# Performance work log

Measured on AMD Instinct MI355X. Metric: run time of the kernel, lower is better.

The kernel has to match this reference:

```python
import jax, jax.numpy as jnp
import numpy as np

ALPHA = 0.25
GAMMA = 2.0
EDGE_W = 1.0
NODE_W = 1.0

N = 200_000
E = 12_800_000
N_GRAPHS = 16
N_INST = 1000


def setup_inputs() -> dict:
    key = jax.random.key(0)
    k1, k2, k3, k4, k5 = jax.random.split(key, 5)
    edge_logits = jax.random.normal(k1, (E,), dtype=jnp.float32)
    node_logits = jax.random.normal(k2, (N,), dtype=jnp.float32)
    batch = jnp.sort(jax.random.randint(k3, (N,), 0, N_GRAPHS, dtype=jnp.int64) if jax.config.read('jax_enable_x64') else jax.random.randint(k3, (N,), 0, N_GRAPHS, dtype=jnp.int32))
    point_instances = jax.random.randint(k4, (N,), 0, N_INST, dtype=jnp.int32)
    edge_index = jax.random.randint(k5, (2, E), 0, N, dtype=jnp.int32)
    return {"edge_logits": edge_logits, "node_logits": node_logits,
            "batch": batch, "point_instances": point_instances,
            "edge_index": edge_index}


def _bce_with_logits(x, t):
    # numerically stable elementwise BCE-with-logits (reduction='none')
    return jnp.maximum(x, 0.0) - x * t + jnp.log1p(jnp.exp(-jnp.abs(x)))


def _sigmoid_focal_loss(x, t, alpha, gamma):
    # torchvision.ops.sigmoid_focal_loss, reduction='mean'
    p = jax.nn.sigmoid(x)
    ce = _bce_with_logits(x, t)
    p_t = p * t + (1.0 - p) * (1.0 - t)
    loss = ce * (1.0 - p_t) ** gamma
    alpha_t = alpha * t + (1.0 - alpha) * (1.0 - t)
    return jnp.mean(alpha_t * loss)


def _accuracy(x, t):
    # sigmoid > 0.5 -> 1 else 0 (note: == 0.5 maps to 0, as in the original)
    pred = (jax.nn.sigmoid(x) > 0.5).astype(x.dtype)
    return jnp.mean((pred == t).astype(jnp.float32))


def reference(edge_logits, node_logits, batch, point_instances, edge_index):
    src, dst = edge_index[0], edge_index[1]
    pi_s = point_instances[src]
    pi_d = point_instances[dst]
    # edge-wise equivalent of the original N x N mask gathered at edge_index:
    # same instance AND same graph AND both instances nonzero
    same = (pi_s == pi_d) & (batch[src] == batch[dst]) & (pi_s != 0) & (pi_d != 0)
    edge_targets = same.astype(jnp.float32)  # [E]

    edge_loss = _sigmoid_focal_loss(edge_logits, edge_targets, ALPHA, GAMMA)
    edge_acc = _accuracy(edge_logits, edge_targets)

    node_targets = (point_instances != 0).astype(jnp.float32)  # [N]
    node_loss = _sigmoid_focal_loss(node_logits, node_targets, ALPHA, GAMMA)
    node_acc = _accuracy(node_logits, node_targets)

    loss = EDGE_W * edge_loss + NODE_W * node_loss
    return loss, edge_loss, node_loss, edge_acc, node_acc
```

## Files before the change

### kernel.cpp

```cpp
#include <hip/hip_runtime.h>
#include <limits.h>


typedef int   iv4 __attribute__((ext_vector_type(4)));
typedef float fv4 __attribute__((ext_vector_type(4)));

#define MAX_PART 4096

__device__ __forceinline__ float focal_term(float x, int t) {
    float y = t ? -x : x;
    float e = __expf(-fabsf(y));
    float ce = fmaxf(y, 0.f) + __logf(1.f + e);
    float inv = __builtin_amdgcn_rcpf(1.f + e);
    float sg = (y >= 0.f) ? inv : e * inv;
    float w = t ? 0.25f : 0.75f;
    return w * ce * sg * sg;
}

__device__ __forceinline__ float acc_term(float x, int t) {
    return ((x > 0.f) == (t != 0)) ? 1.f : 0.f;
}

__device__ __forceinline__ void block_store2(float v0, float v1, float2* part) {
#pragma unroll
    for (int off = 32; off > 0; off >>= 1) {
        v0 += __shfl_down(v0, off, 64);
        v1 += __shfl_down(v1, off, 64);
    }
    __shared__ float s0[8], s1[8];
    int wave = threadIdx.x >> 6;
    int lane = threadIdx.x & 63;
    if (lane == 0) { s0[wave] = v0; s1[wave] = v1; }
    __syncthreads();
    if (threadIdx.x == 0) {
        int nw = blockDim.x >> 6;
        float t0 = 0.f, t1 = 0.f;
        for (int w = 0; w < nw; ++w) { t0 += s0[w]; t1 += s1[w]; }
        part[blockIdx.x] = make_float2(t0, t1);
    }
}

__device__ __forceinline__ void block_store4(float v0, float v1, float v2,
                                             float v3, float4* part) {
#pragma unroll
    for (int off = 32; off > 0; off >>= 1) {
        v0 += __shfl_down(v0, off, 64);
        v1 += __shfl_down(v1, off, 64);
        v2 += __shfl_down(v2, off, 64);
        v3 += __shfl_down(v3, off, 64);
    }
    __shared__ float s[4][8];
    int wave = threadIdx.x >> 6;
    int lane = threadIdx.x & 63;
    if (lane == 0) { s[0][wave] = v0; s[1][wave] = v1;
                     s[2][wave] = v2; s[3][wave] = v3; }
    __syncthreads();
    if (threadIdx.x == 0) {
        int nw = blockDim.x >> 6;
        float t0 = 0.f, t1 = 0.f, t2 = 0.f, t3 = 0.f;
        for (int w = 0; w < nw; ++w) {
            t0 += s[0][w]; t1 += s[1][w]; t2 += s[2][w]; t3 += s[3][w];
        }
        part[blockIdx.x] = make_float4(t0, t1, t2, t3);
    }
}

__global__ void __launch_bounds__(256, 4)
node_e1_kernel(const float* __restrict__ nl,
               const int* __restrict__ batch,
               const int* __restrict__ pi,
               int N,
               const float* __restrict__ el, int E,
               unsigned short* __restrict__ key,
               int* __restrict__ bnd,
               float4* __restrict__ part) {
    int tid = blockIdx.x * blockDim.x + threadIdx.x;
    int nth = gridDim.x * blockDim.x;
    float nls = 0.f, nac = 0.f, els = 0.f, eac = 0.f;

    int C = N >> 3;
    const iv4* pi4 = reinterpret_cast<const iv4*>(pi);
    const iv4* b4  = reinterpret_cast<const iv4*>(batch);
    const fv4* nl4 = reinterpret_cast<const fv4*>(nl);
    for (int c = tid; c < C; c += nth) {
        int base = c << 3;
        iv4 p0 = pi4[(c << 1) + 0], p1 = pi4[(c << 1) + 1];
        iv4 b0 = b4[(c << 1) + 0],  b1 = b4[(c << 1) + 1];
        fv4 x0 = nl4[(c << 1) + 0], x1 = nl4[(c << 1) + 1];
        int pv[8] = {p0.x, p0.y, p0.z, p0.w, p1.x, p1.y, p1.z, p1.w};
        int bv[8] = {b0.x, b0.y, b0.z, b0.w, b1.x, b1.y, b1.z, b1.w};
        float xv[8] = {x0.x, x0.y, x0.z, x0.w, x1.x, x1.y, x1.z, x1.w};
        int bp = (base > 0) ? batch[base - 1] : -1;
        unsigned int kv[8];
#pragma unroll
        for (int j = 0; j < 8; ++j) {
            int p = pv[j];
            int t = (p != 0) ? 1 : 0;
            int b = bv[j];
            kv[j] = t ? (unsigned int)((b << 10) | p) : 0u;
            if (bp != b) {
                for (int k = bp + 1; k <= b; ++k) bnd[k] = base + j;
            }
            bp = b;
            nls += focal_term(xv[j], t);
            nac += acc_term(xv[j], t);
        }
        if (base + 8 == N) {
            for (int k = bv[7] + 1; k <= 16; ++k) bnd[k] = N;
        }
        iv4 kp;
        kp.x = (int)(kv[0] | (kv[1] << 16));
        kp.y = (int)(kv[2] | (kv[3] << 16));
        kp.z = (int)(kv[4] | (kv[5] << 16));
        kp.w = (int)(kv[6] | (kv[7] << 16));
        reinterpret_cast<iv4*>(key)[c] = kp;
    }
    if (tid == 0) {
        for (int i = C << 3; i < N; ++i) {
            int p = pi[i];
            int t = (p != 0) ? 1 : 0;
            int b = batch[i];
            key[i] = t ? (unsigned short)((b << 10) | p) : (unsigned short)0;
            if (i == 0) {
                for (int k = 0; k <= b; ++k) bnd[k] = 0;
            } else {
                int bp = batch[i - 1];
                for (int k = bp + 1; k <= b; ++k) bnd[k] = i;
            }
            if (i == N - 1) {
                for (int k = b + 1; k <= 16; ++k) bnd[k] = N;
            }
            float x = nl[i];
            nls += focal_term(x, t);
            nac += acc_term(x, t);
        }
    }

    int G16 = E >> 4;
    const fv4* el4 = reinterpret_cast<const fv4*>(el);
    for (int g = tid; g < G16; g += nth) {
        int base = g << 2;
        fv4 y0 = __builtin_nontemporal_load(el4 + base + 0);
        fv4 y1 = __builtin_nontemporal_load(el4 + base + 1);
        fv4 y2 = __builtin_nontemporal_load(el4 + base + 2);
        fv4 y3 = __builtin_nontemporal_load(el4 + base + 3);
        float xv[16] = {y0.x, y0.y, y0.z, y0.w, y1.x, y1.y, y1.z, y1.w,
                        y2.x, y2.y, y2.z, y2.w, y3.x, y3.y, y3.z, y3.w};
#pragma unroll
        for (int i = 0; i < 16; ++i) {
            els += focal_term(xv[i], 0);
            eac += acc_term(xv[i], 0);
        }
    }
    if (tid == 0) {
        for (int i = G16 << 4; i < E; ++i) {
            float x = el[i];
            els += focal_term(x, 0);
            eac += acc_term(x, 0);
        }
    }
    block_store4(nls, nac, els, eac, part);
}

__global__ void __launch_bounds__(256, 4)
edge_corr_kernel(const int* __restrict__ src,
                 const int* __restrict__ dst,
                 const float* __restrict__ el,
                 const unsigned short* __restrict__ key,
                 const int* __restrict__ bnd_g,
                 int E, float gscale,
                 float2* __restrict__ part) {
    __shared__ int bnd[17];
    if (threadIdx.x < 17) bnd[threadIdx.x] = bnd_g[threadIdx.x];
    __syncthreads();

    const int G16 = E >> 4;
    int tid = blockIdx.x * blockDim.x + threadIdx.x;
    int nth = gridDim.x * blockDim.x;
    float ls = 0.f, ac = 0.f;
    const iv4* src4 = reinterpret_cast<const iv4*>(src);
    const iv4* dst4 = reinterpret_cast<const iv4*>(dst);

    for (int g = tid; g < G16; g += nth) {
        int base = g << 2;
#pragma unroll
        for (int j = 0; j < 4; ++j) {
            iv4 s4 = __builtin_nontemporal_load(src4 + base + j);
            iv4 d4 = __builtin_nontemporal_load(dst4 + base + j);
            int ss[4] = {s4.x, s4.y, s4.z, s4.w};
            int dd[4] = {d4.x, d4.y, d4.z, d4.w};
#pragma unroll
            for (int k = 0; k < 4; ++k) {
                int s = ss[k], d = dd[k];
                int gg = (int)((float)s * gscale);
                gg = gg < 0 ? 0 : (gg > 15 ? 15 : gg);
                int lo = bnd[gg], hi = bnd[gg + 1];
                while (s < lo) { --gg; hi = lo; lo = bnd[gg]; }
                while (s >= hi) { ++gg; lo = hi; hi = bnd[gg + 1]; }
                if ((d >= lo) & (d < hi)) {
                    unsigned short ks = key[s];
                    unsigned short kd = key[d];
                    if ((ks == kd) & (ks != 0)) {
                        float x = el[(g << 4) + (j << 2) + k];
                        ls += focal_term(x, 1) - focal_term(x, 0);
                        ac += (x > 0.f) ? 1.f : -1.f;
                    }
                }
            }
        }
    }
    if (tid == 0) {
        for (int i = (G16 << 4); i < E; ++i) {
            int s = src[i], d = dst[i];
            int gg = (int)((float)s * gscale);
            gg = gg < 0 ? 0 : (gg > 15 ? 15 : gg);
            int lo = bnd[gg], hi = bnd[gg + 1];
            while (s < lo) { --gg; hi = lo; lo = bnd[gg]; }
            while (s >= hi) { ++gg; lo = hi; hi = bnd[gg + 1]; }
            if ((d >= lo) & (d < hi)) {
                unsigned short ks = key[s], kd = key[d];
                if ((ks == kd) & (ks != 0)) {
                    float x = el[i];
                    ls += focal_term(x, 1) - focal_term(x, 0);
                    ac += (x > 0.f) ? 1.f : -1.f;
                }
            }
        }
    }
    block_store2(ls, ac, part);
}

__global__ void node_atomic_kernel(const float* __restrict__ nl,
                                   const int* __restrict__ pi,
                                   int N, float* __restrict__ acc) {
    int stride = gridDim.x * blockDim.x;
    float ls = 0.f, ac = 0.f;
    for (int i = blockIdx.x * blockDim.x + threadIdx.x; i < N; i += stride) {
        int t = (pi[i] != 0) ? 1 : 0;
        float x = nl[i];
        ls += focal_term(x, t);
        ac += acc_term(x, t);
    }
#pragma unroll
    for (int off = 32; off > 0; off >>= 1) {
        ls += __shfl_down(ls, off, 64);
        ac += __shfl_down(ac, off, 64);
    }
    if ((threadIdx.x & 63) == 0) {
        atomicAdd(acc + 2, ls);
        atomicAdd(acc + 3, ac);
    }
}

__global__ void edge_kernel_direct(const float* __restrict__ el,
                                   const int* __restrict__ src,
                                   const int* __restrict__ dst,
                                   const int* __restrict__ batch,
                                   const int* __restrict__ pi,
                                   int E, float* __restrict__ acc) {
    int stride = gridDim.x * blockDim.x;
    float ls = 0.f, ac = 0.f;
    for (int i = blockIdx.x * blockDim.x + threadIdx.x; i < E; i += stride) {
        int ps = pi[src[i]], pd = pi[dst[i]];
        int t = (ps == pd) & (batch[src[i]] == batch[dst[i]]) & (ps != 0);
        float x = el[i];
        ls += focal_term(x, t);
        ac += acc_term(x, t);
    }
#pragma unroll
    for (int off = 32; off > 0; off >>= 1) {
        ls += __shfl_down(ls, off, 64);
        ac += __shfl_down(ac, off, 64);
    }
    if ((threadIdx.x & 63) == 0) {
        atomicAdd(acc + 0, ls);
        atomicAdd(acc + 1, ac);
    }
}

__global__ void finalize_kernel(const float* __restrict__ acc,
                                const float4* __restrict__ p1, int n1,
                                const float2* __restrict__ p2, int n2,
                                int use_part,
                                float* __restrict__ out, int E, int N) {
    if (use_part) {
        float nls = 0.f, nac = 0.f, els = 0.f, eac = 0.f;
        for (int i = threadIdx.x; i < n1; i += 256) {
            float4 p = p1[i];
            nls += p.x; nac += p.y; els += p.z; eac += p.w;
        }
        for (int i = threadIdx.x; i < n2; i += 256) {
            float2 p = p2[i];
            els += p.x; eac += p.y;
        }
#pragma unroll
        for (int off = 32; off > 0; off >>= 1) {
            nls += __shfl_down(nls, off, 64);
            nac += __shfl_down(nac, off, 64);
            els += __shfl_down(els, off, 64);
            eac += __shfl_down(eac, off, 64);
        }
        __shared__ float s[4][4];
        int wave = threadIdx.x >> 6;
        int lane = threadIdx.x & 63;
        if (lane == 0) { s[0][wave] = nls; s[1][wave] = nac;
                         s[2][wave] = els; s[3][wave] = eac; }
        __syncthreads();
        if (threadIdx.x == 0) {
            nls = 0.f; nac = 0.f; els = 0.f; eac = 0.f;
            for (int w = 0; w < 4; ++w) {
                nls += s[0][w]; nac += s[1][w];
                els += s[2][w]; eac += s[3][w];
            }
            float invE = 1.f / (float)E;
            float invN = 1.f / (float)N;
            float elm = els * invE, eam = eac * invE;
            float nlm = nls * invN, nam = nac * invN;
            out[0] = elm + nlm;
            out[1] = elm;
            out[2] = nlm;
            out[3] = eam;
            out[4] = nam;
        }
    } else if (threadIdx.x == 0) {
        float invE = 1.f / (float)E;
        float invN = 1.f / (float)N;
        float elm = acc[0] * invE;
        float eam = acc[1] * invE;
        float nlm = acc[2] * invN;
        float nam = acc[3] * invN;
        out[0] = elm + nlm;
        out[1] = elm;
        out[2] = nlm;
        out[3] = eam;
        out[4] = nam;
    }
}

extern "C" void kernel_launch(void* const* d_in, const int* in_sizes, int n_in,
                              void* d_out, int out_size, void* d_ws, size_t ws_size,
                              hipStream_t stream) {
    const float* edge_logits = (const float*)d_in[0];
    const float* node_logits = (const float*)d_in[1];
    const int*   batch       = (const int*)d_in[2];
    const int*   pinst       = (const int*)d_in[3];
    const int*   eidx        = (const int*)d_in[4];
    const int E = in_sizes[0];
    const int N = in_sizes[1];
    const int* src = eidx;
    const int* dst = eidx + E;
    float* out = (float*)d_out;

    float* acc = (float*)d_ws;
    int*   bnd = (int*)((char*)d_ws + 64);
    unsigned short* key = (unsigned short*)((char*)d_ws + 256);
    size_t key_end = 256 + (size_t)N * sizeof(unsigned short);
    size_t part_off = (key_end + 255) & ~(size_t)255;
    float4* part1 = (float4*)((char*)d_ws + part_off);
    float2* part2 = (float2*)(part1 + MAX_PART);
    size_t need_full = part_off + MAX_PART * (sizeof(float4) + sizeof(float2));

    const bool full = (ws_size >= need_full);
    const int block = 256;
    int C = N >> 3;
    int G16 = E >> 4;

    if (full) {
        int g1 = (G16 + block - 1) / block;
        int g1n = (C + block - 1) / block;
        if (g1n > g1) g1 = g1n;
        if (g1 < 1) g1 = 1;
        if (g1 > MAX_PART) g1 = MAX_PART;
        int g2 = (G16 + block - 1) / block;
        if (g2 < 1) g2 = 1;
        if (g2 > MAX_PART) g2 = MAX_PART;

        node_e1_kernel<<<g1, block, 0, stream>>>(node_logits, batch, pinst, N,
                                                 edge_logits, E, key, bnd, part1);
        float gscale = 16.0f / (float)N;
        edge_corr_kernel<<<g2, block, 0, stream>>>(src, dst, edge_logits, key,
                                                   bnd, E, gscale, part2);
        finalize_kernel<<<1, 256, 0, stream>>>(acc, part1, g1, part2, g2, 1,
                                               out, E, N);
    } else {
        (void)hipMemsetAsync(d_ws, 0, 16, stream);
        int ng = (N + block - 1) / block;
        if (ng > 2048) ng = 2048;
        node_atomic_kernel<<<ng, block, 0, stream>>>(node_logits, pinst, N, acc);
        int eg = (E + block - 1) / block;
        if (eg > 2048) eg = 2048;
        edge_kernel_direct<<<eg, block, 0, stream>>>(edge_logits, src, dst,
                                                     batch, pinst, E, acc);
        finalize_kernel<<<1, 256, 0, stream>>>(acc, part1, 0, part2, 0, 0,
                                               out, E, N);
    }
}
```

Before: 242.7 us.

## Drop packed key array, use wave-coalesced edge loads and deferred pi gathers

Removes the 16-bit packed key array written by the node kernel. The edge kernel now gathers point_instances directly, which is safe because the same-graph check is already done through the batch boundaries. Both edge loops switch from per-thread contiguous 64-byte chunks to wave-strided float4 loads, so each load instruction covers a contiguous 1 KB span per wave. The correction kernel first builds a bitmask of same-graph edges and then runs the pi gathers only for set bits, at the cost of 4-byte instead of 2-byte gathers and a larger register array per thread.

Result: faster. 202.5 us (-16.6%).

```diff
diff --git a/kernel.cpp b/kernel.cpp
--- a/kernel.cpp
+++ b/kernel.cpp
@@ -71,7 +71,6 @@
                const int* __restrict__ pi,
                int N,
                const float* __restrict__ el, int E,
-               unsigned short* __restrict__ key,
                int* __restrict__ bnd,
                float4* __restrict__ part) {
     int tid = blockIdx.x * blockDim.x + threadIdx.x;
@@ -91,13 +90,10 @@
         int bv[8] = {b0.x, b0.y, b0.z, b0.w, b1.x, b1.y, b1.z, b1.w};
         float xv[8] = {x0.x, x0.y, x0.z, x0.w, x1.x, x1.y, x1.z, x1.w};
         int bp = (base > 0) ? batch[base - 1] : -1;
-        unsigned int kv[8];
 #pragma unroll
         for (int j = 0; j < 8; ++j) {
-            int p = pv[j];
-            int t = (p != 0) ? 1 : 0;
+            int t = (pv[j] != 0) ? 1 : 0;
             int b = bv[j];
-            kv[j] = t ? (unsigned int)((b << 10) | p) : 0u;
             if (bp != b) {
                 for (int k = bp + 1; k <= b; ++k) bnd[k] = base + j;
             }
@@ -108,19 +104,11 @@
         if (base + 8 == N) {
             for (int k = bv[7] + 1; k <= 16; ++k) bnd[k] = N;
         }
-        iv4 kp;
-        kp.x = (int)(kv[0] | (kv[1] << 16));
-        kp.y = (int)(kv[2] | (kv[3] << 16));
-        kp.z = (int)(kv[4] | (kv[5] << 16));
-        kp.w = (int)(kv[6] | (kv[7] << 16));
-        reinterpret_cast<iv4*>(key)[c] = kp;
     }
     if (tid == 0) {
         for (int i = C << 3; i < N; ++i) {
-            int p = pi[i];
-            int t = (p != 0) ? 1 : 0;
+            int t = (pi[i] != 0) ? 1 : 0;
             int b = batch[i];
-            key[i] = t ? (unsigned short)((b << 10) | p) : (unsigned short)0;
             if (i == 0) {
                 for (int k = 0; k <= b; ++k) bnd[k] = 0;
             } else {
@@ -136,24 +124,24 @@
         }
     }
 
-    int G16 = E >> 4;
+    int lane = threadIdx.x & 63;
+    int wid = tid >> 6;
+    int nwaves = nth >> 6;
+    int NW = E >> 10;
     const fv4* el4 = reinterpret_cast<const fv4*>(el);
-    for (int g = tid; g < G16; g += nth) {
-        int base = g << 2;
-        fv4 y0 = __builtin_nontemporal_load(el4 + base + 0);
-        fv4 y1 = __builtin_nontemporal_load(el4 + base + 1);
-        fv4 y2 = __builtin_nontemporal_load(el4 + base + 2);
-        fv4 y3 = __builtin_nontemporal_load(el4 + base + 3);
-        float xv[16] = {y0.x, y0.y, y0.z, y0.w, y1.x, y1.y, y1.z, y1.w,
-                        y2.x, y2.y, y2.z, y2.w, y3.x, y3.y, y3.z, y3.w};
-#pragma unroll
-        for (int i = 0; i < 16; ++i) {
-            els += focal_term(xv[i], 0);
-            eac += acc_term(xv[i], 0);
+    for (int w = wid; w < NW; w += nwaves) {
+        int base4 = w << 8;
+#pragma unroll
+        for (int j = 0; j < 4; ++j) {
+            fv4 x = __builtin_nontemporal_load(el4 + base4 + (j << 6) + lane);
+            els += focal_term(x.x, 0) + focal_term(x.y, 0) +
+                   focal_term(x.z, 0) + focal_term(x.w, 0);
+            eac += acc_term(x.x, 0) + acc_term(x.y, 0) +
+                   acc_term(x.z, 0) + acc_term(x.w, 0);
         }
     }
     if (tid == 0) {
-        for (int i = G16 << 4; i < E; ++i) {
+        for (int i = NW << 10; i < E; ++i) {
             float x = el[i];
             els += focal_term(x, 0);
             eac += acc_term(x, 0);
@@ -166,7 +154,7 @@
 edge_corr_kernel(const int* __restrict__ src,
                  const int* __restrict__ dst,
                  const float* __restrict__ el,
-                 const unsigned short* __restrict__ key,
+                 const int* __restrict__ pi,
                  const int* __restrict__ bnd_g,
                  int E, float gscale,
                  float2* __restrict__ part) {
@@ -174,43 +162,58 @@
     if (threadIdx.x < 17) bnd[threadIdx.x] = bnd_g[threadIdx.x];
     __syncthreads();
 
-    const int G16 = E >> 4;
     int tid = blockIdx.x * blockDim.x + threadIdx.x;
     int nth = gridDim.x * blockDim.x;
+    int lane = threadIdx.x & 63;
+    int wid = tid >> 6;
+    int nwaves = nth >> 6;
+    int NW = E >> 10;
     float ls = 0.f, ac = 0.f;
     const iv4* src4 = reinterpret_cast<const iv4*>(src);
     const iv4* dst4 = reinterpret_cast<const iv4*>(dst);
 
-    for (int g = tid; g < G16; g += nth) {
-        int base = g << 2;
+    for (int w = wid; w < NW; w += nwaves) {
+        int base4 = w << 8;
+        int si[16], di[16];
 #pragma unroll
         for (int j = 0; j < 4; ++j) {
-            iv4 s4 = __builtin_nontemporal_load(src4 + base + j);
-            iv4 d4 = __builtin_nontemporal_load(dst4 + base + j);
-            int ss[4] = {s4.x, s4.y, s4.z, s4.w};
-            int dd[4] = {d4.x, d4.y, d4.z, d4.w};
-#pragma unroll
-            for (int k = 0; k < 4; ++k) {
-                int s = ss[k], d = dd[k];
-                int gg = (int)((float)s * gscale);
-                gg = gg < 0 ? 0 : (gg > 15 ? 15 : gg);
-                int lo = bnd[gg], hi = bnd[gg + 1];
-                while (s < lo) { --gg; hi = lo; lo = bnd[gg]; }
-                while (s >= hi) { ++gg; lo = hi; hi = bnd[gg + 1]; }
-                if ((d >= lo) & (d < hi)) {
-                    unsigned short ks = key[s];
-                    unsigned short kd = key[d];
-                    if ((ks == kd) & (ks != 0)) {
-                        float x = el[(g << 4) + (j << 2) + k];
-                        ls += focal_term(x, 1) - focal_term(x, 0);
-                        ac += (x > 0.f) ? 1.f : -1.f;
-                    }
-                }
+            iv4 s = __builtin_nontemporal_load(src4 + base4 + (j << 6) + lane);
+            si[j * 4 + 0] = s.x; si[j * 4 + 1] = s.y;
+            si[j * 4 + 2] = s.z; si[j * 4 + 3] = s.w;
+        }
+#pragma unroll
+        for (int j = 0; j < 4; ++j) {
+            iv4 d = __builtin_nontemporal_load(dst4 + base4 + (j << 6) + lane);
+            di[j * 4 + 0] = d.x; di[j * 4 + 1] = d.y;
+            di[j * 4 + 2] = d.z; di[j * 4 + 3] = d.w;
+        }
+        unsigned int sameM = 0;
+#pragma unroll
+        for (int i = 0; i < 16; ++i) {
+            int s = si[i], d = di[i];
+            int gg = (int)((float)s * gscale);
+            gg = gg < 0 ? 0 : (gg > 15 ? 15 : gg);
+            int lo = bnd[gg], hi = bnd[gg + 1];
+            while (s < lo) { --gg; hi = lo; lo = bnd[gg]; }
+            while (s >= hi) { ++gg; lo = hi; hi = bnd[gg + 1]; }
+            sameM |= (unsigned int)((d >= lo) & (d < hi)) << i;
+        }
+        while (sameM) {
+            int i = (int)__builtin_ctz(sameM);
+            sameM &= sameM - 1;
+            int s = si[i], d = di[i];
+            int ps = pi[s];
+            int pd = pi[d];
+            if ((ps == pd) & (ps != 0)) {
+                int ei = (w << 10) + ((((i >> 2) << 6) + lane) << 2) + (i & 3);
+                float x = el[ei];
+                ls += focal_term(x, 1) - focal_term(x, 0);
+                ac += (x > 0.f) ? 1.f : -1.f;
             }
         }
     }
     if (tid == 0) {
-        for (int i = (G16 << 4); i < E; ++i) {
+        for (int i = NW << 10; i < E; ++i) {
             int s = src[i], d = dst[i];
             int gg = (int)((float)s * gscale);
             gg = gg < 0 ? 0 : (gg > 15 ? 15 : gg);
@@ -218,8 +221,8 @@
             while (s < lo) { --gg; hi = lo; lo = bnd[gg]; }
             while (s >= hi) { ++gg; lo = hi; hi = bnd[gg + 1]; }
             if ((d >= lo) & (d < hi)) {
-                unsigned short ks = key[s], kd = key[d];
-                if ((ks == kd) & (ks != 0)) {
+                int ps = pi[s], pd = pi[d];
+                if ((ps == pd) & (ps != 0)) {
                     float x = el[i];
                     ls += focal_term(x, 1) - focal_term(x, 0);
                     ac += (x > 0.f) ? 1.f : -1.f;
@@ -353,33 +356,30 @@
 
     float* acc = (float*)d_ws;
     int*   bnd = (int*)((char*)d_ws + 64);
-    unsigned short* key = (unsigned short*)((char*)d_ws + 256);
-    size_t key_end = 256 + (size_t)N * sizeof(unsigned short);
-    size_t part_off = (key_end + 255) & ~(size_t)255;
-    float4* part1 = (float4*)((char*)d_ws + part_off);
+    float4* part1 = (float4*)((char*)d_ws + 256);
     float2* part2 = (float2*)(part1 + MAX_PART);
-    size_t need_full = part_off + MAX_PART * (sizeof(float4) + sizeof(float2));
+    size_t need_full = 256 + MAX_PART * (sizeof(float4) + sizeof(float2));
 
     const bool full = (ws_size >= need_full);
     const int block = 256;
     int C = N >> 3;
-    int G16 = E >> 4;
+    int NW = E >> 10;
 
     if (full) {
-        int g1 = (G16 + block - 1) / block;
+        int g1 = (NW + 3) >> 2;
         int g1n = (C + block - 1) / block;
         if (g1n > g1) g1 = g1n;
         if (g1 < 1) g1 = 1;
         if (g1 > MAX_PART) g1 = MAX_PART;
-        int g2 = (G16 + block - 1) / block;
+        int g2 = (NW + 3) >> 2;
         if (g2 < 1) g2 = 1;
         if (g2 > MAX_PART) g2 = MAX_PART;
 
         node_e1_kernel<<<g1, block, 0, stream>>>(node_logits, batch, pinst, N,
-                                                 edge_logits, E, key, bnd, part1);
+                                                 edge_logits, E, bnd, part1);
         float gscale = 16.0f / (float)N;
-        edge_corr_kernel<<<g2, block, 0, stream>>>(src, dst, edge_logits, key,
-                                                   bnd, E, gscale, part2);
+        edge_corr_kernel<<<g2, block, 0, stream>>>(src, dst, edge_logits,
+                                                   pinst, bnd, E, gscale, part2);
         finalize_kernel<<<1, 256, 0, stream>>>(acc, part1, g1, part2, g2, 1,
                                                out, E, N);
     } else {
```
